# Performance work log

Hardware: AMD Instinct MI355X
Metric: run time of the kernel (lower is better)

Reference implementation:

```python
import jax, jax.numpy as jnp
import numpy as np

B, T, U, V = 8, 256, 64, 512
BLANK = 0


def setup_inputs() -> dict:
    key = jax.random.key(0)
    k1, k2, k3, k4 = jax.random.split(key, 4)
    logits = jax.random.normal(k1, (B, T, U + 1, V), dtype=jnp.float32)
    # labels in [1, V) so they never collide with blank=0
    targets = jax.random.randint(k2, (B, U), 1, V, dtype=jnp.int32)
    logit_lengths = jax.random.randint(k3, (B,), T // 2, T + 1, dtype=jnp.int32)
    target_lengths = jax.random.randint(k4, (B,), U // 2, U + 1, dtype=jnp.int32)
    return {"logits": logits, "targets": targets,
            "logit_lengths": logit_lengths, "target_lengths": target_lengths}


def _logcumsumexp(x, axis):
    # numerically stable cumulative logsumexp via associative scan of logaddexp
    return jax.lax.associative_scan(jnp.logaddexp, x, axis=axis)


def _rnnt_log_likelihood(logits, targets, logit_lengths, target_lengths):
    # logits: [B, T, U+1, V]
    lp = jax.nn.log_softmax(logits, axis=-1)
    lp_blank = lp[..., BLANK]                                        # [B, T, U+1]
    # lp_label[b, t, u] = log P(targets[b, u] | t, u)
    lp_label = jnp.take_along_axis(
        lp[:, :, :U, :], targets[:, None, :, None].astype(jnp.int32), axis=3
    )[..., 0]                                                        # [B, T, U]

    zeros = jnp.zeros((B, 1), lp.dtype)
    # alpha[0, u] = sum_{j<u} lp_label[0, j]
    alpha0 = jnp.concatenate([zeros, jnp.cumsum(lp_label[:, 0, :], axis=1)], axis=1)  # [B, U+1]

    # Row recursion: alpha[t,u] = logaddexp(alpha[t-1,u] + blank(t-1,u),
    #                                        alpha[t,u-1] + label(t,u-1)).
    # Within a row this unrolls to a prefix logsumexp:
    #   alpha[t,u] = logcumsumexp_k (a[k] - c[k])[u] + c[u]
    # with a = alpha[t-1] + lp_blank[t-1], c[u] = sum_{j<u} lp_label[t, j].
    def step(alpha_prev, xs):
        lpb_prev, lpl_t = xs                                         # [B,U+1], [B,U]
        a = alpha_prev + lpb_prev
        c = jnp.concatenate([zeros, jnp.cumsum(lpl_t, axis=1)], axis=1)
        alpha_t = _logcumsumexp(a - c, axis=1) + c
        return alpha_t, alpha_t

    xs = (jnp.swapaxes(lp_blank, 0, 1)[:-1],   # blank probs of rows 0..T-2
          jnp.swapaxes(lp_label, 0, 1)[1:])    # label probs of rows 1..T-1
    _, alphas_rest = jax.lax.scan(step, alpha0, xs)                  # [T-1, B, U+1]
    alphas = jnp.concatenate([alpha0[None], alphas_rest], axis=0)    # [T, B, U+1]

    b = jnp.arange(B)
    t_idx = logit_lengths - 1
    u_idx = target_lengths
    # final blank transition out of node (T_b-1, U_b)
    ll = alphas[t_idx, b, u_idx] + lp_blank[b, t_idx, u_idx]
    return ll


def reference(logits, targets, logit_lengths, target_lengths):
    ll = _rnnt_log_likelihood(logits, targets, logit_lengths, target_lengths)
    return jnp.mean(-ll)  # reduction='mean'
```

## Files before the change

### kernel.cpp

```cpp
#include <hip/hip_runtime.h>
#include <cstddef>

#define BB 8
#define TT 256
#define UU 64
#define VV 512
#define WW 65
#define DMAX 321
#define ROWF 68
#define BSTR (DMAX * ROWF)

#define K2_CHUNK 32
#define K2_CV ((K2_CHUNK * ROWF) / 4)

__device__ __forceinline__ float lae(float a, float b) {
    float m = fmaxf(a, b);
    float d = fminf(a, b) - m;
    return m + log1pf(__expf(d));
}

__global__ __launch_bounds__(256) void rnnt_lse_kernel(
    const float* __restrict__ logits, const int* __restrict__ targets,
    const int* __restrict__ loglen, const int* __restrict__ tgtlen,
    float* __restrict__ lpb, float* __restrict__ lpl) {
    const int wave = (blockIdx.x * blockDim.x + threadIdx.x) >> 6;
    const int lane = threadIdx.x & 63;
    const int ncells = BB * TT * WW;
    if (wave >= ncells) return;
    const int b = wave / (TT * WW);
    int rem = wave - b * (TT * WW);
    const int t = rem / WW;
    const int u = rem - t * WW;
    const int tb = loglen[b];
    const int ub = tgtlen[b];
    if (t >= tb || u > ub) return;

    const float4* src = ((const float4*)logits) + ((size_t)wave << 7) + (lane << 1);
    const float4 va = src[0];
    const float4 vb = src[1];

    float m = fmaxf(fmaxf(fmaxf(va.x, va.y), fmaxf(va.z, va.w)),
                    fmaxf(fmaxf(vb.x, vb.y), fmaxf(vb.z, vb.w)));
    #pragma unroll
    for (int off = 32; off; off >>= 1) m = fmaxf(m, __shfl_xor(m, off));

    float s = expf(va.x - m) + expf(va.y - m) + expf(va.z - m) + expf(va.w - m)
            + expf(vb.x - m) + expf(vb.y - m) + expf(vb.z - m) + expf(vb.w - m);
    #pragma unroll
    for (int off = 32; off; off >>= 1) s += __shfl_xor(s, off);

    const float lse = m + logf(s);
    const int d = t + u + 1;
    const size_t rowbase = (size_t)b * BSTR + (size_t)d * ROWF;

    if (lane == 0) lpb[rowbase + u] = va.x - lse;

    if (u < UU) {
        const int tgt = targets[b * UU + u];
        if (lane == (tgt >> 3)) {
            const int j = tgt & 7;
            float v;
            switch (j) {
                case 0: v = va.x; break; case 1: v = va.y; break;
                case 2: v = va.z; break; case 3: v = va.w; break;
                case 4: v = vb.x; break; case 5: v = vb.y; break;
                case 6: v = vb.z; break; default: v = vb.w; break;
            }
            lpl[rowbase + u + 1] = v - lse;
        }
    }
}

__global__ __launch_bounds__(64) void rnnt_dp_kernel(
    const float* __restrict__ lpb, const float* __restrict__ lpl,
    const int* __restrict__ loglen, const int* __restrict__ tgtlen,
    float* __restrict__ out) {
    __shared__ float4 sb[2][K2_CV];
    __shared__ float4 sl[2][K2_CV];
    const int b = blockIdx.x;
    const int lane = threadIdx.x;
    const int tb = loglen[b];
    const int ub = tgtlen[b];
    const int d_final = tb - 1 + ub;
    const size_t bbase = (size_t)b * BSTR;
    const float4* gb = (const float4*)(lpb + bbase);
    const float4* gl = (const float4*)(lpl + bbase);

    float4 rb[9], rl[9];

    #pragma unroll
    for (int j = 0; j < 9; ++j) {
        const int idx = j * 64 + lane;
        if (idx < K2_CV) { rb[j] = gb[idx]; rl[j] = gl[idx]; }
    }
    #pragma unroll
    for (int j = 0; j < 9; ++j) {
        const int idx = j * 64 + lane;
        if (idx < K2_CV) { sb[0][idx] = rb[j]; sl[0][idx] = rl[j]; }
    }
    __syncthreads();

    const int nch = d_final / K2_CHUNK + 1;
    int cur = 0;
    float al = -1e30f;
    float a0 = 0.0f;
    float cap = 0.0f;

    for (int k = 0; k < nch; ++k) {
        const bool pref = (k + 1 < nch);
        if (pref) {
            const int off = (k + 1) * K2_CV;
            #pragma unroll
            for (int j = 0; j < 9; ++j) {
                const int idx = j * 64 + lane;
                if (idx < K2_CV) { rb[j] = gb[off + idx]; rl[j] = gl[off + idx]; }
            }
        }
        const float* cb = (const float*)sb[cur];
        const float* cl = (const float*)sl[cur];
        const int dlo = (k == 0) ? 1 : k * K2_CHUNK;
        const int dhi = min(d_final, k * K2_CHUNK + K2_CHUNK - 1);
        for (int dd = dlo; dd <= dhi; ++dd) {
            const int r = dd - k * K2_CHUNK;
            const float bv = cb[r * ROWF + lane + 1];
            const float lv = cl[r * ROWF + lane + 1];
            const float b0 = cb[r * ROWF];
            float a_prev = __shfl_up(al, 1);
            if (lane == 0) a_prev = a0;
            const float x = al + bv;
            const float y = a_prev + lv;
            al = (lane + 1 == dd) ? y : lae(x, y);
            a0 += b0;
            if (dd == d_final) cap = al;
        }
        if (pref) {
            #pragma unroll
            for (int j = 0; j < 9; ++j) {
                const int idx = j * 64 + lane;
                if (idx < K2_CV) { sb[cur ^ 1][idx] = rb[j]; sl[cur ^ 1][idx] = rl[j]; }
            }
        }
        __syncthreads();
        cur ^= 1;
    }

    if (lane == ub - 1) {
        const float lpbf = lpb[bbase + (size_t)(d_final + 1) * ROWF + ub];
        atomicAdd(out, -0.125f * (cap + lpbf));
    }
}

extern "C" void kernel_launch(void* const* d_in, const int* in_sizes, int n_in,
                              void* d_out, int out_size, void* d_ws, size_t ws_size,
                              hipStream_t stream) {
    const float* logits = (const float*)d_in[0];
    const int* targets  = (const int*)d_in[1];
    const int* loglen   = (const int*)d_in[2];
    const int* tgtlen   = (const int*)d_in[3];
    float* out = (float*)d_out;

    float* lpb = (float*)d_ws;
    float* lpl = lpb + (size_t)BB * BSTR;

    hipMemsetAsync(d_out, 0, sizeof(float), stream);

    const int ncells = BB * TT * WW;
    const int blocks = ncells / 4;
    hipLaunchKernelGGL(rnnt_lse_kernel, dim3(blocks), dim3(256), 0, stream,
                       logits, targets, loglen, tgtlen, lpb, lpl);
    hipLaunchKernelGGL(rnnt_dp_kernel, dim3(BB), dim3(64), 0, stream,
                       lpb, lpl, loglen, tgtlen, out);
}
```

Baseline: 456.3 us.

## Use base-2 log domain, drop softmax max pass, DPP shift and unrolled DP loop

```diff
diff --git a/kernel.cpp b/kernel.cpp
--- a/kernel.cpp
+++ b/kernel.cpp
@@ -13,10 +13,21 @@
 #define K2_CHUNK 32
 #define K2_CV ((K2_CHUNK * ROWF) / 4)
 
-__device__ __forceinline__ float lae(float a, float b) {
+#define INVLN2 1.4426950408889634f
+#define LN2    0.6931471805599453f
+
+__device__ __forceinline__ float hw_exp2(float x) { return __builtin_amdgcn_exp2f(x); }
+
+__device__ __forceinline__ float lae2(float a, float b) {
     float m = fmaxf(a, b);
     float d = fminf(a, b) - m;
-    return m + log1pf(__expf(d));
+    return m + __log2f(1.0f + hw_exp2(d));
+}
+
+__device__ __forceinline__ float dpp_shr1(float x) {
+    int xi = __builtin_bit_cast(int, x);
+    int r = __builtin_amdgcn_update_dpp(xi, xi, 0x138 , 0xF, 0xF, false);
+    return __builtin_bit_cast(float, r);
 }
 
 __global__ __launch_bounds__(256) void rnnt_lse_kernel(
@@ -25,48 +36,36 @@
     float* __restrict__ lpb, float* __restrict__ lpl) {
     const int wave = (blockIdx.x * blockDim.x + threadIdx.x) >> 6;
     const int lane = threadIdx.x & 63;
-    const int ncells = BB * TT * WW;
-    if (wave >= ncells) return;
     const int b = wave / (TT * WW);
     int rem = wave - b * (TT * WW);
     const int t = rem / WW;
     const int u = rem - t * WW;
-    const int tb = loglen[b];
-    const int ub = tgtlen[b];
-    if (t >= tb || u > ub) return;
+    if (t >= loglen[b] || u > tgtlen[b]) return;
 
-    const float4* src = ((const float4*)logits) + ((size_t)wave << 7) + (lane << 1);
-    const float4 va = src[0];
-    const float4 vb = src[1];
+    const float4* src = ((const float4*)logits) + ((size_t)wave << 7);
+    const float4 va = src[lane];
+    const float4 vb = src[lane + 64];
 
-    float m = fmaxf(fmaxf(fmaxf(va.x, va.y), fmaxf(va.z, va.w)),
-                    fmaxf(fmaxf(vb.x, vb.y), fmaxf(vb.z, vb.w)));
-    #pragma unroll
-    for (int off = 32; off; off >>= 1) m = fmaxf(m, __shfl_xor(m, off));
-
-    float s = expf(va.x - m) + expf(va.y - m) + expf(va.z - m) + expf(va.w - m)
-            + expf(vb.x - m) + expf(vb.y - m) + expf(vb.z - m) + expf(vb.w - m);
+    float s = __expf(va.x) + __expf(va.y) + __expf(va.z) + __expf(va.w)
+            + __expf(vb.x) + __expf(vb.y) + __expf(vb.z) + __expf(vb.w);
     #pragma unroll
     for (int off = 32; off; off >>= 1) s += __shfl_xor(s, off);
 
-    const float lse = m + logf(s);
+    const float lse2 = __log2f(s);
     const int d = t + u + 1;
     const size_t rowbase = (size_t)b * BSTR + (size_t)d * ROWF;
 
-    if (lane == 0) lpb[rowbase + u] = va.x - lse;
+    if (lane == 0)
+        lpb[rowbase + u] = __builtin_fmaf(va.x, INVLN2, -lse2);
 
     if (u < UU) {
         const int tgt = targets[b * UU + u];
-        if (lane == (tgt >> 3)) {
-            const int j = tgt & 7;
-            float v;
-            switch (j) {
-                case 0: v = va.x; break; case 1: v = va.y; break;
-                case 2: v = va.z; break; case 3: v = va.w; break;
-                case 4: v = vb.x; break; case 5: v = vb.y; break;
-                case 6: v = vb.z; break; default: v = vb.w; break;
-            }
-            lpl[rowbase + u + 1] = v - lse;
+        const bool hi = tgt >= 256;
+        if (lane == ((tgt >> 2) & 63)) {
+            const float4 v = hi ? vb : va;
+            const int j = tgt & 3;
+            const float x = (j == 0) ? v.x : (j == 1) ? v.y : (j == 2) ? v.z : v.w;
+            lpl[rowbase + u + 1] = __builtin_fmaf(x, INVLN2, -lse2);
         }
     }
 }
@@ -118,19 +117,21 @@
         }
         const float* cb = (const float*)sb[cur];
         const float* cl = (const float*)sl[cur];
-        const int dlo = (k == 0) ? 1 : k * K2_CHUNK;
-        const int dhi = min(d_final, k * K2_CHUNK + K2_CHUNK - 1);
-        for (int dd = dlo; dd <= dhi; ++dd) {
-            const int r = dd - k * K2_CHUNK;
+        const int dbase = k * K2_CHUNK;
+        #pragma unroll 8
+        for (int r = 0; r < K2_CHUNK; ++r) {
+            const int dd = dbase + r;
             const float bv = cb[r * ROWF + lane + 1];
             const float lv = cl[r * ROWF + lane + 1];
             const float b0 = cb[r * ROWF];
-            float a_prev = __shfl_up(al, 1);
+            float a_prev = dpp_shr1(al);
             if (lane == 0) a_prev = a0;
             const float x = al + bv;
             const float y = a_prev + lv;
-            al = (lane + 1 == dd) ? y : lae(x, y);
-            a0 += b0;
+            const float nal = (lane + 1 == dd) ? y : lae2(x, y);
+            const bool valid = (dd >= 1) && (dd <= d_final);
+            al = valid ? nal : al;
+            a0 = valid ? a0 + b0 : a0;
             if (dd == d_final) cap = al;
         }
         if (pref) {
@@ -146,7 +147,7 @@
 
     if (lane == ub - 1) {
         const float lpbf = lpb[bbase + (size_t)(d_final + 1) * ROWF + ub];
-        atomicAdd(out, -0.125f * (cap + lpbf));
+        atomicAdd(out, -0.125f * LN2 * (cap + lpbf));
     }
 }
 
@@ -162,7 +163,7 @@
     float* lpb = (float*)d_ws;
     float* lpl = lpb + (size_t)BB * BSTR;
 
-    hipMemsetAsync(d_out, 0, sizeof(float), stream);
+    (void)hipMemsetAsync(d_out, 0, sizeof(float), stream);
 
     const int ncells = BB * TT * WW;
     const int blocks = ncells / 4;
```

After: 403.9 us. -11.5%, faster.
